# Performance work log

Measured on AMD Instinct MI355X. Metric: run time of the kernel, lower is better.

The kernel has to match this reference:

```python
import jax, jax.numpy as jnp
import numpy as np

B, D, K, U = 4096, 1024, 5, 1024  # batch, input_dim, num_basis, units


def setup_inputs() -> dict:
    key = jax.random.key(0)
    k1, k2, k3 = jax.random.split(key, 3)
    x = jax.random.normal(k1, (B, D), dtype=jnp.float32)
    basis_weights = jax.random.normal(k2, (D, K, U), dtype=jnp.float32) * 0.02
    bias = jax.random.normal(k3, (U,), dtype=jnp.float32) * 0.02
    return {"x": x, "basis_weights": basis_weights, "bias": bias}


def reference(x, basis_weights, bias):
    # Polynomial basis expansion: x^0, x^1, ..., x^{K-1}  -> (B, D, K)
    num_basis = basis_weights.shape[1]
    powers = jnp.arange(num_basis, dtype=x.dtype)
    basis = x[..., None] ** powers  # x**0 == 1, matching tf.ones_like branch
    # Fused: einsum('bik,ikj->bij') followed by reduce_sum over i == 'bik,ikj->bj'.
    # Avoids materializing the (B, D, U) intermediate of the original.
    out = jnp.einsum("bik,ikj->bj", basis, basis_weights) + bias
    # tf.nn.gelu defaults to exact (non-approximate) GELU.
    return jax.nn.gelu(out, approximate=False)
```

## Files before the change

### kernel.cpp

```cpp
#include <hip/hip_runtime.h>
#include <hip/hip_bf16.h>
#include <math.h>


#define B_DIM 4096
#define D_DIM 1024
#define U_DIM 1024
#define NKB 128

typedef unsigned short ushort_t;
typedef __attribute__((ext_vector_type(8))) short bf16x8;
typedef __attribute__((ext_vector_type(4))) float f32x4;
typedef __attribute__((ext_vector_type(2))) float f32x2;

__device__ __forceinline__ ushort_t f2bf(float f) {
  union { float f; unsigned int u; } v;
  v.f = f;
  unsigned int r = v.u + 0x7FFFu + ((v.u >> 16) & 1u);
  return (ushort_t)(r >> 16);
}

__device__ __forceinline__ void load_lds16(const ushort_t* g, ushort_t* l) {
  __builtin_amdgcn_global_load_lds(
      (const __attribute__((address_space(1))) ushort_t*)g,
      (__attribute__((address_space(3))) ushort_t*)l, 16, 0, 0);
}

__device__ __forceinline__ float gelu_exact(float v) {
  return 0.5f * v * (1.0f + erff(v * 0.70710678118654752f));
}


__global__ __launch_bounds__(256) void prep_kernel(
    const float* __restrict__ x, const float* __restrict__ W,
    float* __restrict__ Xp, ushort_t* __restrict__ Bp,
    float* __restrict__ fold8) {
  __shared__ __align__(16) float lsh[64][132];

  const int bid  = blockIdx.x;
  const int t    = threadIdx.x;
  const int wave = t >> 6;
  const int lane = t & 63;
  const int m    = lane & 15;
  const int ko   = lane >> 4;

  if (bid < 512) {
    const int mt = bid >> 3;
    const int g  = bid & 7;
    const float* xbase = x + (size_t)mt * 64 * D_DIM + g * 128;
#pragma unroll
    for (int p = 0; p < 8; ++p) {
      const int row = p * 8 + wave * 2 + (lane >> 5);
      const int c4  = lane & 31;
      *(float4*)&lsh[row][c4 * 4] =
          *(const float4*)(xbase + (size_t)row * D_DIM + c4 * 4);
    }
    __syncthreads();
#pragma unroll
    for (int r = 0; r < 4; ++r) {
      const int itl = r * 4 + wave;
      const int it  = g * 16 + itl;
      float* dst = Xp + ((size_t)(mt * NKB + it)) * 512 + lane * 8;
      float f[8];
#pragma unroll
      for (int j = 0; j < 8; ++j) f[j] = lsh[lane][itl * 8 + j];
      *(float4*)(dst)     = *(const float4*)&f[0];
      *(float4*)(dst + 4) = *(const float4*)&f[4];
    }
  } else {
    const int wid = bid - 512;
    const int n16 = wid >> 3;
    const int kg  = wid & 7;
    const int j   = n16 * 16 + m;
    float s0 = 0.0f;
#pragma unroll
    for (int kk = 0; kk < 4; ++kk) {
      const int kblk = kg * 16 + kk * 4 + wave;
      const int i0   = kblk * 8 + ko * 2;
      ushort_t o[8];
#pragma unroll
      for (int t2 = 0; t2 < 2; ++t2) {
        const int i = i0 + t2;
        s0 += W[(size_t)(i * 5) * U_DIM + j];
#pragma unroll
        for (int e = 0; e < 4; ++e)
          o[t2 * 4 + e] = f2bf(W[(size_t)(i * 5 + e + 1) * U_DIM + j]);
      }
      *(uint4*)(Bp + ((size_t)n16 * NKB + kblk) * 512 + lane * 8) =
          *(const uint4*)o;
    }
    s0 += __shfl_xor(s0, 16, 64);
    s0 += __shfl_xor(s0, 32, 64);
    float* red = &lsh[0][0];
    if (ko == 0) red[wave * 16 + m] = s0;
    __syncthreads();
    if (wave == 0 && ko == 0)
      fold8[(size_t)kg * U_DIM + j] =
          red[m] + red[16 + m] + red[32 + m] + red[48 + m];
  }
}

__global__ __launch_bounds__(256) void gemm_kernel(
    const float* __restrict__ Xp, const ushort_t* __restrict__ Bp,
    const float* __restrict__ bias, const float* __restrict__ fold8,
    float* __restrict__ C) {
  __shared__ __align__(16) ushort_t lds[4][5120];

  const int tid  = threadIdx.x;
  const int wave = tid >> 6;
  const int lane = tid & 63;
  const int wm   = wave >> 1;
  const int wn   = wave & 1;

  const int lin  = blockIdx.y * 8 + blockIdx.x;
  const int xcd  = lin & 7;
  const int slot = lin >> 3;
  const int mt   = xcd * 8 + (slot & 7);
  const int nt   = slot >> 3;
  const int m16b = mt * 4;
  const int n16b = nt * 8;

  const ushort_t* gx  = (const ushort_t*)(Xp + (size_t)mt * NKB * 512) + lane * 8;
  const ushort_t* gb0 = Bp + ((size_t)(n16b + wave) * NKB) * 512 + lane * 8;
  const ushort_t* gb1 = Bp + ((size_t)(n16b + 4 + wave) * NKB) * 512 + lane * 8;
  const int ldx0 = lane * 8;
  const int ldx1 = 512 + lane * 8;
  const int ldb0 = 1024 + wave * 512 + lane * 8;
  const int ldb1 = 1024 + (4 + wave) * 512 + lane * 8;

  f32x4 acc[2][4];
  const f32x4 zero = {0.0f, 0.0f, 0.0f, 0.0f};
#pragma unroll
  for (int mf = 0; mf < 2; ++mf)
#pragma unroll
    for (int nf = 0; nf < 4; ++nf) acc[mf][nf] = zero;

#define WAITBAR(N) \
  asm volatile("s_waitcnt vmcnt(" #N ")\n\ts_barrier" ::: "memory")

#define STAGE_REL(bb, rel)                                              \
  do {                                                                  \
    load_lds16(gx  + (rel) * 1024,       &lds[bb][ldx0]);               \
    load_lds16(gx  + (rel) * 1024 + 512, &lds[bb][ldx1]);               \
    load_lds16(gb0 + (rel) * 512,        &lds[bb][ldb0]);               \
    load_lds16(gb1 + (rel) * 512,        &lds[bb][ldb1]);               \
  } while (0)

#define PACKA(dst, xp)                                                  \
  do {                                                                  \
    const f32x2 p1 = (xp);                                              \
    const f32x2 p2 = p1 * p1;                                           \
    const f32x2 p3 = p2 * p1;                                           \
    const f32x2 p4 = p2 * p2;                                           \
    bf16x8 rr;                                                          \
    rr[0] = (short)f2bf(p1[0]); rr[1] = (short)f2bf(p2[0]);             \
    rr[2] = (short)f2bf(p3[0]); rr[3] = (short)f2bf(p4[0]);             \
    rr[4] = (short)f2bf(p1[1]); rr[5] = (short)f2bf(p2[1]);             \
    rr[6] = (short)f2bf(p3[1]); rr[7] = (short)f2bf(p4[1]);             \
    dst = rr;                                                           \
  } while (0)

#define COMPUTE(bb)                                                     \
  do {                                                                  \
    const float* xu = (const float*)&lds[bb][0];                        \
    f32x2 xp0 = *(const f32x2*)&xu[((wm * 2 + 0) * 16 + (lane & 15)) * 8 + (lane >> 4) * 2]; \
    f32x2 xp1 = *(const f32x2*)&xu[((wm * 2 + 1) * 16 + (lane & 15)) * 8 + (lane >> 4) * 2]; \
    bf16x8 a[2], b[4];                                                  \
    PACKA(a[0], xp0);                                                   \
    PACKA(a[1], xp1);                                                   \
    _Pragma("unroll")                                                   \
    for (int nf = 0; nf < 4; ++nf)                                      \
      b[nf] = *(const bf16x8*)&lds[bb][1024 + (wn * 4 + nf) * 512 + lane * 8]; \
    _Pragma("unroll")                                                   \
    for (int mf = 0; mf < 2; ++mf)                                      \
      _Pragma("unroll")                                                 \
      for (int nf = 0; nf < 4; ++nf)                                    \
        acc[mf][nf] = __builtin_amdgcn_mfma_f32_16x16x32_bf16(          \
            a[mf], b[nf], acc[mf][nf], 0, 0, 0);                        \
  } while (0)

  STAGE_REL(0, 0);
  STAGE_REL(1, 1);
  STAGE_REL(2, 2);
  gx  += 4 * 1024;
  gb0 += 4 * 512;
  gb1 += 4 * 512;

  for (int base = 0; base < 124; base += 4) {
    WAITBAR(8); STAGE_REL(3, -1); COMPUTE(0);
    WAITBAR(8); STAGE_REL(0,  0); COMPUTE(1);
    WAITBAR(8); STAGE_REL(1,  1); COMPUTE(2);
    WAITBAR(8); STAGE_REL(2,  2); COMPUTE(3);
    gx  += 4 * 1024;
    gb0 += 4 * 512;
    gb1 += 4 * 512;
  }
  WAITBAR(8); STAGE_REL(3, -1); COMPUTE(0);
  WAITBAR(8); COMPUTE(1);
  WAITBAR(4); COMPUTE(2);
  WAITBAR(0); COMPUTE(3);
#undef STAGE_REL
#undef COMPUTE
#undef PACKA
#undef WAITBAR

  const int crow0 = m16b * 16 + wm * 32 + (lane >> 4) * 4;
  const int ccol0 = n16b * 16 + wn * 64 + (lane & 15);
#pragma unroll
  for (int nf = 0; nf < 4; ++nf) {
    const int col = ccol0 + nf * 16;
    float bv = bias[col];
#pragma unroll
    for (int kg = 0; kg < 8; ++kg) bv += fold8[(size_t)kg * U_DIM + col];
#pragma unroll
    for (int mf = 0; mf < 2; ++mf) {
#pragma unroll
      for (int r = 0; r < 4; ++r) {
        const int row = crow0 + mf * 16 + r;
        C[(size_t)row * U_DIM + col] = gelu_exact(acc[mf][nf][r] + bv);
      }
    }
  }
}

__global__ void fallback_kernel(const float* __restrict__ x, const float* __restrict__ W,
                                const float* __restrict__ bias, float* __restrict__ out) {
  int j  = blockIdx.x * 256 + threadIdx.x;
  int b0 = blockIdx.y * 16;
  float acc[16];
#pragma unroll
  for (int t = 0; t < 16; ++t) acc[t] = 0.0f;
  for (int i = 0; i < D_DIM; ++i) {
    const float* wr = W + (size_t)i * 5 * U_DIM + j;
    float w0 = wr[0 * U_DIM], w1 = wr[1 * U_DIM], w2 = wr[2 * U_DIM];
    float w3 = wr[3 * U_DIM], w4 = wr[4 * U_DIM];
#pragma unroll
    for (int t = 0; t < 16; ++t) {
      float xv = x[(size_t)(b0 + t) * D_DIM + i];
      float x2 = xv * xv;
      acc[t] += w0 + xv * w1 + x2 * w2 + x2 * xv * w3 + x2 * x2 * w4;
    }
  }
  float bv = bias[j];
#pragma unroll
  for (int t = 0; t < 16; ++t)
    out[(size_t)(b0 + t) * U_DIM + j] = gelu_exact(acc[t] + bv);
}

extern "C" void kernel_launch(void* const* d_in, const int* in_sizes, int n_in,
                              void* d_out, int out_size, void* d_ws, size_t ws_size,
                              hipStream_t stream) {
  const float* x    = (const float*)d_in[0];
  const float* W    = (const float*)d_in[1];
  const float* bias = (const float*)d_in[2];
  float* out = (float*)d_out;

  const size_t szX = (size_t)B_DIM * D_DIM * sizeof(float);
  const size_t szB = (size_t)U_DIM * 4096 * sizeof(ushort_t);
  const size_t szF = (size_t)8 * U_DIM * sizeof(float);

  if (ws_size >= szX + szB + szF) {
    float*    Xp = (float*)d_ws;
    ushort_t* Bp = (ushort_t*)((char*)d_ws + szX);
    float*    f8 = (float*)((char*)d_ws + szX + szB);
    prep_kernel<<<dim3(1024), 256, 0, stream>>>(x, W, Xp, Bp, f8);
    gemm_kernel<<<dim3(U_DIM / 128, B_DIM / 64), 256, 0, stream>>>(Xp, Bp, bias, f8, out);
  } else {
    fallback_kernel<<<dim3(U_DIM / 256, B_DIM / 16), 256, 0, stream>>>(x, W, bias, out);
  }
}
```

Baseline: 149.6 us.

## Load x directly into LDS with swizzle, drop x repack pass

```diff
diff --git a/kernel.cpp b/kernel.cpp
--- a/kernel.cpp
+++ b/kernel.cpp
@@ -30,78 +30,48 @@
   return 0.5f * v * (1.0f + erff(v * 0.70710678118654752f));
 }
 
-
-__global__ __launch_bounds__(256) void prep_kernel(
-    const float* __restrict__ x, const float* __restrict__ W,
-    float* __restrict__ Xp, ushort_t* __restrict__ Bp,
+__global__ __launch_bounds__(256) void w_pack_kernel(
+    const float* __restrict__ W, ushort_t* __restrict__ Bp,
     float* __restrict__ fold8) {
-  __shared__ __align__(16) float lsh[64][132];
-
-  const int bid  = blockIdx.x;
+  __shared__ float red[64];
+  const int wid  = blockIdx.x;
   const int t    = threadIdx.x;
   const int wave = t >> 6;
   const int lane = t & 63;
   const int m    = lane & 15;
   const int ko   = lane >> 4;
-
-  if (bid < 512) {
-    const int mt = bid >> 3;
-    const int g  = bid & 7;
-    const float* xbase = x + (size_t)mt * 64 * D_DIM + g * 128;
-#pragma unroll
-    for (int p = 0; p < 8; ++p) {
-      const int row = p * 8 + wave * 2 + (lane >> 5);
-      const int c4  = lane & 31;
-      *(float4*)&lsh[row][c4 * 4] =
-          *(const float4*)(xbase + (size_t)row * D_DIM + c4 * 4);
+  const int n16  = wid >> 3;
+  const int kg   = wid & 7;
+  const int j    = n16 * 16 + m;
+
+  float s0 = 0.0f;
+#pragma unroll
+  for (int kk = 0; kk < 4; ++kk) {
+    const int kblk = kg * 16 + kk * 4 + wave;
+    const int i0   = kblk * 8 + ko * 2;
+    ushort_t o[8];
+#pragma unroll
+    for (int t2 = 0; t2 < 2; ++t2) {
+      const int i = i0 + t2;
+      s0 += W[(size_t)(i * 5) * U_DIM + j];
+#pragma unroll
+      for (int e = 0; e < 4; ++e)
+        o[t2 * 4 + e] = f2bf(W[(size_t)(i * 5 + e + 1) * U_DIM + j]);
     }
-    __syncthreads();
-#pragma unroll
-    for (int r = 0; r < 4; ++r) {
-      const int itl = r * 4 + wave;
-      const int it  = g * 16 + itl;
-      float* dst = Xp + ((size_t)(mt * NKB + it)) * 512 + lane * 8;
-      float f[8];
-#pragma unroll
-      for (int j = 0; j < 8; ++j) f[j] = lsh[lane][itl * 8 + j];
-      *(float4*)(dst)     = *(const float4*)&f[0];
-      *(float4*)(dst + 4) = *(const float4*)&f[4];
-    }
-  } else {
-    const int wid = bid - 512;
-    const int n16 = wid >> 3;
-    const int kg  = wid & 7;
-    const int j   = n16 * 16 + m;
-    float s0 = 0.0f;
-#pragma unroll
-    for (int kk = 0; kk < 4; ++kk) {
-      const int kblk = kg * 16 + kk * 4 + wave;
-      const int i0   = kblk * 8 + ko * 2;
-      ushort_t o[8];
-#pragma unroll
-      for (int t2 = 0; t2 < 2; ++t2) {
-        const int i = i0 + t2;
-        s0 += W[(size_t)(i * 5) * U_DIM + j];
-#pragma unroll
-        for (int e = 0; e < 4; ++e)
-          o[t2 * 4 + e] = f2bf(W[(size_t)(i * 5 + e + 1) * U_DIM + j]);
-      }
-      *(uint4*)(Bp + ((size_t)n16 * NKB + kblk) * 512 + lane * 8) =
-          *(const uint4*)o;
-    }
-    s0 += __shfl_xor(s0, 16, 64);
-    s0 += __shfl_xor(s0, 32, 64);
-    float* red = &lsh[0][0];
-    if (ko == 0) red[wave * 16 + m] = s0;
-    __syncthreads();
-    if (wave == 0 && ko == 0)
-      fold8[(size_t)kg * U_DIM + j] =
-          red[m] + red[16 + m] + red[32 + m] + red[48 + m];
-  }
+    *(uint4*)(Bp + ((size_t)n16 * NKB + kblk) * 512 + lane * 8) =
+        *(const uint4*)o;
+  }
+  s0 += __shfl_xor(s0, 16, 64);
+  s0 += __shfl_xor(s0, 32, 64);
+  if (ko == 0) red[wave * 16 + m] = s0;
+  __syncthreads();
+  if (wave == 0 && ko == 0)
+    fold8[(size_t)kg * U_DIM + j] =
+        red[m] + red[16 + m] + red[32 + m] + red[48 + m];
 }
 
 __global__ __launch_bounds__(256) void gemm_kernel(
-    const float* __restrict__ Xp, const ushort_t* __restrict__ Bp,
+    const float* __restrict__ x, const ushort_t* __restrict__ Bp,
     const float* __restrict__ bias, const float* __restrict__ fold8,
     float* __restrict__ C) {
   __shared__ __align__(16) ushort_t lds[4][5120];
@@ -111,6 +81,8 @@
   const int lane = tid & 63;
   const int wm   = wave >> 1;
   const int wn   = wave & 1;
+  const int m    = lane & 15;
+  const int ko   = lane >> 4;
 
   const int lin  = blockIdx.y * 8 + blockIdx.x;
   const int xcd  = lin & 7;
@@ -120,14 +92,20 @@
   const int m16b = mt * 4;
   const int n16b = nt * 8;
 
-  const ushort_t* gx  = (const ushort_t*)(Xp + (size_t)mt * NKB * 512) + lane * 8;
+  const int xrow  = (wave & 1) * 32 + (lane >> 1);
+  const int xchk  = (lane & 1) ^ ((lane >> 3) & 1);
+  const ushort_t* gx =
+      (const ushort_t*)(x + ((size_t)(m16b * 16 + xrow)) * D_DIM + xchk * 4);
+  const int ldx = (wave & 1) * 512 + lane * 8;
+
   const ushort_t* gb0 = Bp + ((size_t)(n16b + wave) * NKB) * 512 + lane * 8;
   const ushort_t* gb1 = Bp + ((size_t)(n16b + 4 + wave) * NKB) * 512 + lane * 8;
-  const int ldx0 = lane * 8;
-  const int ldx1 = 512 + lane * 8;
   const int ldb0 = 1024 + wave * 512 + lane * 8;
   const int ldb1 = 1024 + (4 + wave) * 512 + lane * 8;
 
+  const int xoff = wm * 1024 + m * 32 +
+                   ((((ko >> 1) ^ ((m >> 2) & 1))) << 4) + (ko & 1) * 8;
+
   f32x4 acc[2][4];
   const f32x4 zero = {0.0f, 0.0f, 0.0f, 0.0f};
 #pragma unroll
@@ -140,10 +118,9 @@
 
 #define STAGE_REL(bb, rel)                                              \
   do {                                                                  \
-    load_lds16(gx  + (rel) * 1024,       &lds[bb][ldx0]);               \
-    load_lds16(gx  + (rel) * 1024 + 512, &lds[bb][ldx1]);               \
-    load_lds16(gb0 + (rel) * 512,        &lds[bb][ldb0]);               \
-    load_lds16(gb1 + (rel) * 512,        &lds[bb][ldb1]);               \
+    load_lds16(gx  + (rel) * 16,  &lds[bb][ldx]);                       \
+    load_lds16(gb0 + (rel) * 512, &lds[bb][ldb0]);                      \
+    load_lds16(gb1 + (rel) * 512, &lds[bb][ldb1]);                      \
   } while (0)
 
 #define PACKA(dst, xp)                                                  \
@@ -152,22 +129,22 @@
     const f32x2 p2 = p1 * p1;                                           \
     const f32x2 p3 = p2 * p1;                                           \
     const f32x2 p4 = p2 * p2;                                           \
-    bf16x8 rr;                                                          \
-    rr[0] = (short)f2bf(p1[0]); rr[1] = (short)f2bf(p2[0]);             \
-    rr[2] = (short)f2bf(p3[0]); rr[3] = (short)f2bf(p4[0]);             \
-    rr[4] = (short)f2bf(p1[1]); rr[5] = (short)f2bf(p2[1]);             \
-    rr[6] = (short)f2bf(p3[1]); rr[7] = (short)f2bf(p4[1]);             \
-    dst = rr;                                                           \
+    union { bf16x8 v; unsigned int u[4]; } r_;                          \
+    asm("v_cvt_pk_bf16_f32 %0, %1, %2" : "=v"(r_.u[0]) : "v"(p1[0]), "v"(p2[0])); \
+    asm("v_cvt_pk_bf16_f32 %0, %1, %2" : "=v"(r_.u[1]) : "v"(p3[0]), "v"(p4[0])); \
+    asm("v_cvt_pk_bf16_f32 %0, %1, %2" : "=v"(r_.u[2]) : "v"(p1[1]), "v"(p2[1])); \
+    asm("v_cvt_pk_bf16_f32 %0, %1, %2" : "=v"(r_.u[3]) : "v"(p3[1]), "v"(p4[1])); \
+    dst = r_.v;                                                         \
   } while (0)
 
 #define COMPUTE(bb)                                                     \
   do {                                                                  \
-    const float* xu = (const float*)&lds[bb][0];                        \
-    f32x2 xp0 = *(const f32x2*)&xu[((wm * 2 + 0) * 16 + (lane & 15)) * 8 + (lane >> 4) * 2]; \
-    f32x2 xp1 = *(const f32x2*)&xu[((wm * 2 + 1) * 16 + (lane & 15)) * 8 + (lane >> 4) * 2]; \
+    const char* xu = (const char*)&lds[bb][0];                          \
+    const f32x2 q0 = *(const f32x2*)(xu + xoff);                        \
+    const f32x2 q1 = *(const f32x2*)(xu + xoff + 512);                  \
     bf16x8 a[2], b[4];                                                  \
-    PACKA(a[0], xp0);                                                   \
-    PACKA(a[1], xp1);                                                   \
+    PACKA(a[0], q0);                                                    \
+    PACKA(a[1], q1);                                                    \
     _Pragma("unroll")                                                   \
     for (int nf = 0; nf < 4; ++nf)                                      \
       b[nf] = *(const bf16x8*)&lds[bb][1024 + (wn * 4 + nf) * 512 + lane * 8]; \
@@ -182,22 +159,22 @@
   STAGE_REL(0, 0);
   STAGE_REL(1, 1);
   STAGE_REL(2, 2);
-  gx  += 4 * 1024;
+  gx  += 4 * 16;
   gb0 += 4 * 512;
   gb1 += 4 * 512;
 
   for (int base = 0; base < 124; base += 4) {
-    WAITBAR(8); STAGE_REL(3, -1); COMPUTE(0);
-    WAITBAR(8); STAGE_REL(0,  0); COMPUTE(1);
-    WAITBAR(8); STAGE_REL(1,  1); COMPUTE(2);
-    WAITBAR(8); STAGE_REL(2,  2); COMPUTE(3);
-    gx  += 4 * 1024;
+    WAITBAR(6); STAGE_REL(3, -1); COMPUTE(0);
+    WAITBAR(6); STAGE_REL(0,  0); COMPUTE(1);
+    WAITBAR(6); STAGE_REL(1,  1); COMPUTE(2);
+    WAITBAR(6); STAGE_REL(2,  2); COMPUTE(3);
+    gx  += 4 * 16;
     gb0 += 4 * 512;
     gb1 += 4 * 512;
   }
-  WAITBAR(8); STAGE_REL(3, -1); COMPUTE(0);
-  WAITBAR(8); COMPUTE(1);
-  WAITBAR(4); COMPUTE(2);
+  WAITBAR(6); STAGE_REL(3, -1); COMPUTE(0);
+  WAITBAR(6); COMPUTE(1);
+  WAITBAR(3); COMPUTE(2);
   WAITBAR(0); COMPUTE(3);
 #undef STAGE_REL
 #undef COMPUTE
@@ -255,16 +232,14 @@
   const float* bias = (const float*)d_in[2];
   float* out = (float*)d_out;
 
-  const size_t szX = (size_t)B_DIM * D_DIM * sizeof(float);
   const size_t szB = (size_t)U_DIM * 4096 * sizeof(ushort_t);
   const size_t szF = (size_t)8 * U_DIM * sizeof(float);
 
-  if (ws_size >= szX + szB + szF) {
-    float*    Xp = (float*)d_ws;
-    ushort_t* Bp = (ushort_t*)((char*)d_ws + szX);
-    float*    f8 = (float*)((char*)d_ws + szX + szB);
-    prep_kernel<<<dim3(1024), 256, 0, stream>>>(x, W, Xp, Bp, f8);
-    gemm_kernel<<<dim3(U_DIM / 128, B_DIM / 64), 256, 0, stream>>>(Xp, Bp, bias, f8, out);
+  if (ws_size >= szB + szF) {
+    ushort_t* Bp = (ushort_t*)d_ws;
+    float*    f8 = (float*)((char*)d_ws + szB);
+    w_pack_kernel<<<dim3(512), 256, 0, stream>>>(W, Bp, f8);
+    gemm_kernel<<<dim3(U_DIM / 128, B_DIM / 64), 256, 0, stream>>>(x, Bp, bias, f8, out);
   } else {
     fallback_kernel<<<dim3(U_DIM / 256, B_DIM / 16), 256, 0, stream>>>(x, W, bias, out);
   }
```

New measurement: 132.4 us. 11.5% less time.
